# Kernel optimization log

Hardware: AMD Instinct MI355X
Metric: run time of the kernel (lower is better)

## Reference

```python
import jax, jax.numpy as jnp
import numpy as np

NEG_SLOPE = 0.2  # PyG GATConv leaky_relu slope


def _gat_layer(x, src, dst, W, a_src, a_dst, b, concat, num_nodes):
    # x: [N, F_in], W: [F_in, H*C], a_src/a_dst: [H, C], b: [H*C] or [C]
    H, C = a_src.shape
    h = (x @ W).reshape(num_nodes, H, C)                      # [N, H, C]
    s_src = jnp.einsum('nhc,hc->nh', h, a_src)                # [N, H]
    s_dst = jnp.einsum('nhc,hc->nh', h, a_dst)                # [N, H]
    e = jax.nn.leaky_relu(s_src[src] + s_dst[dst], NEG_SLOPE) # [E, H]
    # segment softmax over edges sharing a destination node
    m = jax.ops.segment_max(e, dst, num_segments=num_nodes)
    m = jnp.where(jnp.isfinite(m), m, 0.0)
    p = jnp.exp(e - m[dst])
    z = jax.ops.segment_sum(p, dst, num_segments=num_nodes)
    alpha = p / (z[dst] + 1e-16)                              # [E, H]
    msg = h[src] * alpha[:, :, None]                          # [E, H, C]
    out = jax.ops.segment_sum(msg, dst, num_segments=num_nodes)  # [N, H, C]
    out = out.reshape(num_nodes, H * C) if concat else out.mean(axis=1)
    return out + b


def setup_inputs() -> dict:
    key = jax.random.key(0)
    ks = jax.random.split(key, 16)
    N, E, F = 100000, 800000, 128
    H, C = 4, 32
    sc_in = 1.0 / np.sqrt(F)
    inp = {
        'x': jax.random.normal(ks[0], (N, F), jnp.float32),
        'edge_index': jax.random.randint(ks[1], (2, E), 0, N, jnp.int64),
        'W1': jax.random.normal(ks[2], (F, H * C), jnp.float32) * sc_in,
        'a_src1': jax.random.normal(ks[3], (H, C), jnp.float32),
        'a_dst1': jax.random.normal(ks[4], (H, C), jnp.float32),
        'b1': jax.random.normal(ks[5], (H * C,), jnp.float32) * 0.01,
        'W2': jax.random.normal(ks[6], (F, H * C), jnp.float32) * sc_in,
        'a_src2': jax.random.normal(ks[7], (H, C), jnp.float32),
        'a_dst2': jax.random.normal(ks[8], (H, C), jnp.float32),
        'b2': jax.random.normal(ks[9], (H * C,), jnp.float32) * 0.01,
        'W3': jax.random.normal(ks[10], (F, H * F), jnp.float32) * sc_in,
        'a_src3': jax.random.normal(ks[11], (H, F), jnp.float32),
        'a_dst3': jax.random.normal(ks[12], (H, F), jnp.float32),
        'b3': jax.random.normal(ks[13], (F,), jnp.float32) * 0.01,
    }
    return inp


def reference(x, edge_index, W1, a_src1, a_dst1, b1, W2, a_src2, a_dst2, b2,
              W3, a_src3, a_dst3, b3):
    N = x.shape[0]
    # PyG GATConv default: add self loops
    loop = jnp.arange(N, dtype=edge_index.dtype)
    src = jnp.concatenate([edge_index[0], loop])
    dst = jnp.concatenate([edge_index[1], loop])
    # conv1 (concat heads) + residual + ELU
    x1 = jax.nn.elu(_gat_layer(x, src, dst, W1, a_src1, a_dst1, b1, True, N) + x)
    # intermediate conv (concat heads) + residual + ELU
    x2 = jax.nn.elu(_gat_layer(x1, src, dst, W2, a_src2, a_dst2, b2, True, N) + x1)
    # final conv (mean over heads) + residual, no ELU
    x3 = _gat_layer(x2, src, dst, W3, a_src3, a_dst3, b3, False, N) + x2
    return x3
```

## Files before the change

kernel.cpp:

```cpp
#include <hip/hip_runtime.h>
#include <hip/hip_bf16.h>
#include <cstdint>

#define NEG_SLOPE 0.2f

typedef __bf16 bf16x8 __attribute__((ext_vector_type(8)));
typedef _Float16 half8 __attribute__((ext_vector_type(8)));
typedef float  floatx4 __attribute__((ext_vector_type(4)));

__device__ __forceinline__ float us2f(unsigned short u) {
    union { unsigned int i; float f; } c; c.i = ((unsigned int)u) << 16; return c.f;
}
__device__ __forceinline__ unsigned short f2us(float f) {
    union { float f; unsigned int i; } c; c.f = f;
    unsigned int x = c.i;
    unsigned int r = (x + 0x7fffu + ((x >> 16) & 1u)) >> 16;
    return (unsigned short)r;
}
__device__ __forceinline__ unsigned short f2h(float f) {
    union { _Float16 h; unsigned short u; } c; c.h = (_Float16)f; return c.u;
}
__device__ __forceinline__ float h2f(unsigned short u) {
    union { _Float16 h; unsigned short u; } c; c.u = u; return (float)c.h;
}
__device__ __forceinline__ float ldx(const void* p, int i, int bf) {
    return bf ? us2f(((const unsigned short*)p)[i]) : ((const float*)p)[i];
}
__device__ __forceinline__ void split2(float f, unsigned short& h, unsigned short& l) {
    h = f2us(f);
    l = f2us(f - us2f(h));
}
__device__ __forceinline__ float sel4(const float* a, int i) {
    float lo = (i & 1) ? a[1] : a[0];
    float hi = (i & 1) ? a[3] : a[2];
    return (i & 2) ? hi : lo;
}
__device__ __forceinline__ void unp8(uint4 u, float* f) {
    union { unsigned int i; float ff; } a;
    a.i = u.x << 16;          f[0] = a.ff;
    a.i = u.x & 0xffff0000u;  f[1] = a.ff;
    a.i = u.y << 16;          f[2] = a.ff;
    a.i = u.y & 0xffff0000u;  f[3] = a.ff;
    a.i = u.z << 16;          f[4] = a.ff;
    a.i = u.z & 0xffff0000u;  f[5] = a.ff;
    a.i = u.w << 16;          f[6] = a.ff;
    a.i = u.w & 0xffff0000u;  f[7] = a.ff;
}

__global__ void k_detect(const unsigned short* __restrict__ x16,
                         const unsigned int* __restrict__ ei,
                         int* __restrict__ flags) {
    if (threadIdx.x == 0 && blockIdx.x == 0) {
        int cnt = 0;
        for (int i = 0; i < 1024; ++i) {
            const unsigned short u = x16[2 * i];
            const int e = (u >> 7) & 0xFF;
            if (e < 100 || e > 160) ++cnt;
        }
        flags[0] = (cnt < 256) ? 1 : 0;
        int is64 = 1;
        for (int i = 0; i < 64; ++i)
            if (ei[2 * i + 1] != 0u) { is64 = 0; break; }
        flags[1] = is64;
    }
}

__device__ __forceinline__ int edge_at(const void* ei, int f64, long long idx) {
    if (f64) return (int)((const long long*)ei)[idx];
    return ((const int*)ei)[idx];
}

__global__ void k_hist(const void* __restrict__ ei, const int* __restrict__ flags,
                       int* __restrict__ deg, int E, int N) {
    const int f64 = flags[1];
    const int EP = E + N;
    for (int e = blockIdx.x * blockDim.x + threadIdx.x; e < EP; e += gridDim.x * blockDim.x) {
        int dst = (e < E) ? edge_at(ei, f64, (long long)E + e) : (e - E);
        atomicAdd(&deg[dst], 1);
    }
}

__global__ __launch_bounds__(1024) void k_scan_a(const int* __restrict__ deg,
                                                 int* __restrict__ coff,
                                                 int* __restrict__ part, int N) {
    __shared__ int tmp[1024];
    const int t = threadIdx.x, idx = blockIdx.x * 1024 + t;
    const int v = (idx < N) ? deg[idx] : 0;
    tmp[t] = v; __syncthreads();
    for (int s = 1; s < 1024; s <<= 1) {
        int a = (t >= s) ? tmp[t - s] : 0;
        __syncthreads(); tmp[t] += a; __syncthreads();
    }
    if (idx < N) coff[idx] = tmp[t] - v;
    if (t == 1023) part[blockIdx.x] = tmp[1023];
}

__global__ __launch_bounds__(1024) void k_scan_b(int* __restrict__ part,
                                                 int* __restrict__ coff, int nblk, int N) {
    __shared__ int tmp[1024];
    const int t = threadIdx.x;
    const int v = (t < nblk) ? part[t] : 0;
    tmp[t] = v; __syncthreads();
    for (int s = 1; s < 1024; s <<= 1) {
        int a = (t >= s) ? tmp[t - s] : 0;
        __syncthreads(); tmp[t] += a; __syncthreads();
    }
    if (t < nblk) part[t] = tmp[t] - v;
    if (t == 1023) coff[N] = tmp[1023];
}

__global__ __launch_bounds__(1024) void k_scan_c(int* __restrict__ coff,
                                                 const int* __restrict__ part, int N) {
    const int idx = blockIdx.x * 1024 + threadIdx.x;
    if (idx < N) coff[idx] += part[blockIdx.x];
}

__global__ void k_scatter(const void* __restrict__ ei, const int* __restrict__ flags,
                          const int* __restrict__ coff, int* __restrict__ cpos,
                          int* __restrict__ csrc, int E, int N) {
    const int f64 = flags[1];
    const int EP = E + N;
    for (int e = blockIdx.x * blockDim.x + threadIdx.x; e < EP; e += gridDim.x * blockDim.x) {
        int src, dst;
        if (e < E) { src = edge_at(ei, f64, e); dst = edge_at(ei, f64, (long long)E + e); }
        else       { src = dst = e - E; }
        const int p = atomicAdd(&cpos[dst], 1);
        csrc[coff[dst] + p] = src;
    }
}

template <int F16>
__global__ void k_wfrag(const void* __restrict__ Wv, const int* __restrict__ flags,
                        int wstride, int total,
                        unsigned short* __restrict__ outH, unsigned short* __restrict__ outL) {
    const int bf = flags[0];
    for (int tid = blockIdx.x * blockDim.x + threadIdx.x; tid < total;
         tid += gridDim.x * blockDim.x) {
        const int j    = tid & 7;
        const int lane = (tid >> 3) & 63;
        const int ks   = (tid >> 9) & 3;
        const int ntg  = (tid >> 11) & 7;
        const int blk  = tid >> 14;
        const int k = ks * 32 + (lane >> 4) * 8 + j;
        const int c = blk * 128 + ntg * 16 + (lane & 15);
        const float v = ldx(Wv, k * wstride + c, bf);
        unsigned short h, l;
        if (F16) {
            h = f2h(v);
            l = f2h(v - h2f(h));
        } else {
            split2(v, h, l);
        }
        outH[tid] = h; outL[tid] = l;
    }
}

__global__ void k_wa(const void* __restrict__ W, const void* __restrict__ as,
                     const void* __restrict__ ad, const int* __restrict__ flags,
                     float* __restrict__ va) {
    const int bf = flags[0];
    const int t = blockIdx.x * blockDim.x + threadIdx.x;
    if (t >= 512) return;
    const int k = t >> 2, h = t & 3;
    float ss = 0.f, dd = 0.f;
    for (int c = 0; c < 128; ++c) {
        const float w = ldx(W, k * 512 + h * 128 + c, bf);
        ss = fmaf(w, ldx(as, h * 128 + c, bf), ss);
        dd = fmaf(w, ldx(ad, h * 128 + c, bf), dd);
    }
    va[k * 8 + h] = ss;
    va[k * 8 + 4 + h] = dd;
}

template <bool XRAW, int SC>
__global__ __launch_bounds__(256) void k_gemm(const void* __restrict__ Xv,
                                              const unsigned short* __restrict__ whfB,
                                              const unsigned short* __restrict__ wlfB,
                                              unsigned short* __restrict__ Y16, int ystride,
                                              float* __restrict__ ssrc,
                                              float* __restrict__ sdst,
                                              const void* __restrict__ a_src,
                                              const void* __restrict__ a_dst,
                                              const int* __restrict__ flags,
                                              int N) {
    __shared__ __align__(16) unsigned short Ah[64][136], Al[64][136];
    __shared__ float sred[2][4][SC ? 64 : 1];
    const int bf   = flags[0];
    const int t    = threadIdx.x;
    const int row0 = blockIdx.x * 64;
    const int hy   = blockIdx.y;
    const unsigned short* whf = whfB + hy * 16384;
    const unsigned short* wlf = wlfB + hy * 16384;
    const int ycol0 = hy * 128;
    const int wv   = t >> 6;
    const int lane = t & 63;
    const int quad = lane >> 4;
    const int l16  = lane & 15;

#pragma unroll
    for (int it = 0; it < 8; ++it) {
        const int id = it * 256 + t;
        const int r  = id >> 5;
        const int c  = (id & 31) * 4;
        const int gr = row0 + r;
        ushort4 h4 = make_ushort4(0, 0, 0, 0), l4 = make_ushort4(0, 0, 0, 0);
        if (gr < N) {
            if (XRAW && bf) {
                h4 = *(const ushort4*)&((const unsigned short*)Xv)[(size_t)gr * 128 + c];
            } else {
                const float4 f = *(const float4*)&((const float*)Xv)[(size_t)gr * 128 + c];
                split2(f.x, h4.x, l4.x); split2(f.y, h4.y, l4.y);
                split2(f.z, h4.z, l4.z); split2(f.w, h4.w, l4.w);
            }
        }
        *(ushort4*)&Ah[r][c] = h4;
        *(ushort4*)&Al[r][c] = l4;
    }
    __syncthreads();

    floatx4 acc[4][2];
#pragma unroll
    for (int mt = 0; mt < 4; ++mt)
#pragma unroll
        for (int nt = 0; nt < 2; ++nt) acc[mt][nt] = (floatx4){0.f, 0.f, 0.f, 0.f};

#pragma unroll
    for (int ks = 0; ks < 4; ++ks) {
        const int ko = ks * 32 + quad * 8;
        bf16x8 ah[4], al[4], bh[2], bl[2];
#pragma unroll
        for (int mt = 0; mt < 4; ++mt) ah[mt] = *(const bf16x8*)&Ah[mt * 16 + l16][ko];
        if (!(XRAW && bf)) {
#pragma unroll
            for (int mt = 0; mt < 4; ++mt) al[mt] = *(const bf16x8*)&Al[mt * 16 + l16][ko];
        }
#pragma unroll
        for (int nt = 0; nt < 2; ++nt)
            bh[nt] = *(const bf16x8*)&whf[(((wv * 2 + nt) * 4 + ks) * 64 + lane) * 8];
        if (!bf) {
#pragma unroll
            for (int nt = 0; nt < 2; ++nt)
                bl[nt] = *(const bf16x8*)&wlf[(((wv * 2 + nt) * 4 + ks) * 64 + lane) * 8];
        }
#pragma unroll
        for (int mt = 0; mt < 4; ++mt)
#pragma unroll
            for (int nt = 0; nt < 2; ++nt) {
                acc[mt][nt] = __builtin_amdgcn_mfma_f32_16x16x32_bf16(ah[mt], bh[nt], acc[mt][nt], 0, 0, 0);
                if (!bf)
                    acc[mt][nt] = __builtin_amdgcn_mfma_f32_16x16x32_bf16(ah[mt], bl[nt], acc[mt][nt], 0, 0, 0);
                if (!(XRAW && bf))
                    acc[mt][nt] = __builtin_amdgcn_mfma_f32_16x16x32_bf16(al[mt], bh[nt], acc[mt][nt], 0, 0, 0);
            }
    }

    const int aBase = hy * 128 + wv * 32;
    float as_[2], ad_[2];
#pragma unroll
    for (int nt = 0; nt < 2; ++nt) {
        as_[nt] = ldx(a_src, aBase + nt * 16 + l16, bf);
        ad_[nt] = ldx(a_dst, aBase + nt * 16 + l16, bf);
    }

#pragma unroll
    for (int mt = 0; mt < 4; ++mt) {
        const int rl = mt * 16 + quad * 4;
#pragma unroll
        for (int r = 0; r < 4; ++r) {
            const int grow = row0 + rl + r;
            if (grow < N) {
#pragma unroll
                for (int nt = 0; nt < 2; ++nt)
                    Y16[(size_t)grow * ystride + ycol0 + wv * 32 + nt * 16 + l16] =
                        f2us(acc[mt][nt][r]);
            }
            float ps = acc[mt][0][r] * as_[0] + acc[mt][1][r] * as_[1];
            float pd = acc[mt][0][r] * ad_[0] + acc[mt][1][r] * ad_[1];
#pragma unroll
            for (int mk = 1; mk <= 8; mk <<= 1) {
                ps += __shfl_xor(ps, mk);
                pd += __shfl_xor(pd, mk);
            }
            if (SC == 0) {
                if (l16 == 0 && grow < N) {
                    ssrc[(size_t)grow * 4 + wv] = ps;
                    sdst[(size_t)grow * 4 + wv] = pd;
                }
            } else {
                if (l16 == 0) { sred[0][wv][rl + r] = ps; sred[1][wv][rl + r] = pd; }
            }
        }
    }
    if (SC == 1) {
        __syncthreads();
        if (t < 64 && row0 + t < N) {
            ssrc[(size_t)(row0 + t) * 4 + hy] = sred[0][0][t] + sred[0][1][t] + sred[0][2][t] + sred[0][3][t];
            sdst[(size_t)(row0 + t) * 4 + hy] = sred[1][0][t] + sred[1][1][t] + sred[1][2][t] + sred[1][3][t];
        }
    }
}

template <int MODE>
__global__ __launch_bounds__(256) void k_agg(const int* __restrict__ coff,
                                             const int* __restrict__ csrc,
                                             const float* __restrict__ ssrc,
                                             const float* __restrict__ sdst,
                                             const unsigned short* __restrict__ H16,
                                             const void* __restrict__ bias,
                                             const void* __restrict__ resid,
                                             const int* __restrict__ flags,
                                             void* __restrict__ out, int N,
                                             const float* __restrict__ va,
                                             float* __restrict__ ss2,
                                             float* __restrict__ sd2,
                                             unsigned short* __restrict__ x2h) {
    __shared__ float vaS[(MODE == 1) ? 128 : 1][10];
    const int bf   = flags[0];
    const int t    = threadIdx.x;
    const int l16  = t & 15;
    const int n0   = blockIdx.x * 16 + (t >> 4);
    const bool nact = n0 < N;
    const int n    = nact ? n0 : (N - 1);
    const int beg = coff[n], end = coff[n + 1];
    const int deg = end - beg;

    if (MODE == 1) {
        for (int i = t; i < 1024; i += 256) vaS[i >> 3][i & 7] = va[i];
        __syncthreads();
    }

    const float4 sdv = *(const float4*)&sdst[(size_t)n * 4];
    const float sd[4] = { sdv.x, sdv.y, sdv.z, sdv.w };
    const bool fast = (deg <= 16);
    float z[4];
    int   myS = 0;
    float wn[4] = { 0.f, 0.f, 0.f, 0.f };

    if (fast) {
        const bool act = l16 < deg;
        if (act) {
            myS = csrc[beg + l16];
            const float4 sp = *(const float4*)&ssrc[(size_t)myS * 4];
            const float s4[4] = { sp.x, sp.y, sp.z, sp.w };
#pragma unroll
            for (int h = 0; h < 4; ++h) {
                float tv = s4[h] + sd[h];
                tv = tv >= 0.f ? tv : NEG_SLOPE * tv;
                wn[h] = __expf(fminf(tv, 80.f));
            }
        }
#pragma unroll
        for (int h = 0; h < 4; ++h) z[h] = wn[h];
#pragma unroll
        for (int mk = 1; mk <= 8; mk <<= 1)
#pragma unroll
            for (int h = 0; h < 4; ++h) z[h] += __shfl_xor(z[h], mk);
    } else {
#pragma unroll
        for (int h = 0; h < 4; ++h) z[h] = 0.f;
        for (int e = beg + l16; e < end; e += 16) {
            const int s = csrc[e];
            const float4 sp = *(const float4*)&ssrc[(size_t)s * 4];
            const float s4[4] = { sp.x, sp.y, sp.z, sp.w };
#pragma unroll
            for (int h = 0; h < 4; ++h) {
                float tv = s4[h] + sd[h];
                tv = tv >= 0.f ? tv : NEG_SLOPE * tv;
                z[h] += __expf(fminf(tv, 80.f));
            }
        }
#pragma unroll
        for (int mk = 1; mk <= 8; mk <<= 1)
#pragma unroll
            for (int h = 0; h < 4; ++h) z[h] += __shfl_xor(z[h], mk);
    }

    float ivz[4];
#pragma unroll
    for (int h = 0; h < 4; ++h) ivz[h] = 1.f / (z[h] + 1e-16f);

    const int c8 = l16 * 8;
    const int hd = l16 >> 2;
    const float ih = sel4(ivz, hd);
    float ac[8];
#pragma unroll
    for (int j = 0; j < 8; ++j) ac[j] = 0.f;

    if (fast) {
        for (int e = 0; e < deg; ++e) {
            const int s = __shfl(myS, e, 16);
            float wa4[4];
            wa4[0] = __shfl(wn[0], e, 16);
            wa4[1] = __shfl(wn[1], e, 16);
            wa4[2] = __shfl(wn[2], e, 16);
            wa4[3] = __shfl(wn[3], e, 16);
            const float w = sel4(wa4, hd);
            const uint4 u = *(const uint4*)&H16[(size_t)s * 128 + c8];
            float f[8]; unp8(u, f);
#pragma unroll
            for (int j = 0; j < 8; ++j) ac[j] = fmaf(w, f[j], ac[j]);
        }
    } else {
        const float sdh = sel4(sd, hd);
        for (int e = beg; e < end; ++e) {
            const int s = csrc[e];
            float tv = ssrc[(size_t)s * 4 + hd] + sdh;
            tv = tv >= 0.f ? tv : NEG_SLOPE * tv;
            const float w = __expf(fminf(tv, 80.f));
            const uint4 u = *(const uint4*)&H16[(size_t)s * 128 + c8];
            float f[8]; unp8(u, f);
#pragma unroll
            for (int j = 0; j < 8; ++j) ac[j] = fmaf(w, f[j], ac[j]);
        }
    }

#pragma unroll
    for (int j = 0; j < 8; ++j) ac[j] *= ih;

    if (!nact) return;
    const int ob = n * 128 + c8;
    float rr[8];
    if (MODE == 0) {
        if (bf) {
            const uint4 u = *(const uint4*)&((const unsigned short*)resid)[ob];
            unp8(u, rr);
        } else {
            const float4 r0 = *(const float4*)&((const float*)resid)[ob];
            const float4 r1 = *(const float4*)&((const float*)resid)[ob + 4];
            rr[0] = r0.x; rr[1] = r0.y; rr[2] = r0.z; rr[3] = r0.w;
            rr[4] = r1.x; rr[5] = r1.y; rr[6] = r1.z; rr[7] = r1.w;
        }
    } else {
        const float4 r0 = *(const float4*)&((const float*)resid)[ob];
        const float4 r1 = *(const float4*)&((const float*)resid)[ob + 4];
        rr[0] = r0.x; rr[1] = r0.y; rr[2] = r0.z; rr[3] = r0.w;
        rr[4] = r1.x; rr[5] = r1.y; rr[6] = r1.z; rr[7] = r1.w;
    }
    float o[8];
#pragma unroll
    for (int j = 0; j < 8; ++j) {
        const float v = ac[j] + ldx(bias, c8 + j, bf) + rr[j];
        o[j] = v > 0.f ? v : expm1f(v);
    }
    *(float4*)&((float*)out)[ob]     = make_float4(o[0], o[1], o[2], o[3]);
    *(float4*)&((float*)out)[ob + 4] = make_float4(o[4], o[5], o[6], o[7]);

    if (MODE == 1) {
        uint4 u16;
        u16.x = (unsigned int)f2us(o[0]) | ((unsigned int)f2us(o[1]) << 16);
        u16.y = (unsigned int)f2us(o[2]) | ((unsigned int)f2us(o[3]) << 16);
        u16.z = (unsigned int)f2us(o[4]) | ((unsigned int)f2us(o[5]) << 16);
        u16.w = (unsigned int)f2us(o[6]) | ((unsigned int)f2us(o[7]) << 16);
        *(uint4*)&x2h[ob] = u16;
        float p[8];
#pragma unroll
        for (int o8 = 0; o8 < 8; ++o8) {
            float acc = 0.f;
#pragma unroll
            for (int j = 0; j < 8; ++j) acc = fmaf(o[j], vaS[c8 + j][o8], acc);
            p[o8] = acc;
        }
#pragma unroll
        for (int mk = 1; mk <= 8; mk <<= 1)
#pragma unroll
            for (int o8 = 0; o8 < 8; ++o8) p[o8] += __shfl_xor(p[o8], mk);
        if (l16 == 0) {
#pragma unroll
            for (int h = 0; h < 4; ++h) {
                ss2[(size_t)n * 4 + h] = p[h];
                sd2[(size_t)n * 4 + h] = p[4 + h];
            }
        }
    }
}

__global__ __launch_bounds__(256) void k_aggx(const int* __restrict__ coff,
                                              const int* __restrict__ csrc,
                                              const float* __restrict__ ssrc,
                                              const float* __restrict__ sdst,
                                              const unsigned short* __restrict__ X16,
                                              unsigned short* __restrict__ aggO,
                                              int N) {
    const int t    = threadIdx.x;
    const int l16  = t & 15;
    const int n0   = blockIdx.x * 16 + (t >> 4);
    const bool nact = n0 < N;
    const int n    = nact ? n0 : (N - 1);
    const int beg = coff[n], end = coff[n + 1];
    const int deg = end - beg;

    const float4 sdv = *(const float4*)&sdst[(size_t)n * 4];
    const float sd[4] = { sdv.x, sdv.y, sdv.z, sdv.w };
    const bool fast = (deg <= 16);
    float m[4], z[4];
    int   myS = 0;
    float wn[4] = { 0.f, 0.f, 0.f, 0.f };

    if (fast) {
        const bool act = l16 < deg;
        float v[4];
#pragma unroll
        for (int h = 0; h < 4; ++h) v[h] = -1e30f;
        if (act) {
            myS = csrc[beg + l16];
            const float4 sp = *(const float4*)&ssrc[(size_t)myS * 4];
            const float s4[4] = { sp.x, sp.y, sp.z, sp.w };
#pragma unroll
            for (int h = 0; h < 4; ++h) {
                float tv = s4[h] + sd[h];
                v[h] = tv >= 0.f ? tv : NEG_SLOPE * tv;
            }
        }
#pragma unroll
        for (int h = 0; h < 4; ++h) m[h] = v[h];
#pragma unroll
        for (int mk = 1; mk <= 8; mk <<= 1)
#pragma unroll
            for (int h = 0; h < 4; ++h) m[h] = fmaxf(m[h], __shfl_xor(m[h], mk));
        float w[4];
#pragma unroll
        for (int h = 0; h < 4; ++h) w[h] = act ? __expf(v[h] - m[h]) : 0.f;
#pragma unroll
        for (int h = 0; h < 4; ++h) z[h] = w[h];
#pragma unroll
        for (int mk = 1; mk <= 8; mk <<= 1)
#pragma unroll
            for (int h = 0; h < 4; ++h) z[h] += __shfl_xor(z[h], mk);
#pragma unroll
        for (int h = 0; h < 4; ++h) wn[h] = w[h] / (z[h] + 1e-16f);
    } else {
#pragma unroll
        for (int h = 0; h < 4; ++h) m[h] = -1e30f;
        for (int e = beg + l16; e < end; e += 16) {
            const int s = csrc[e];
            const float4 sp = *(const float4*)&ssrc[(size_t)s * 4];
            const float s4[4] = { sp.x, sp.y, sp.z, sp.w };
#pragma unroll
            for (int h = 0; h < 4; ++h) {
                float tv = s4[h] + sd[h];
                tv = tv >= 0.f ? tv : NEG_SLOPE * tv;
                m[h] = fmaxf(m[h], tv);
            }
        }
#pragma unroll
        for (int mk = 1; mk <= 8; mk <<= 1)
#pragma unroll
            for (int h = 0; h < 4; ++h) m[h] = fmaxf(m[h], __shfl_xor(m[h], mk));
#pragma unroll
        for (int h = 0; h < 4; ++h) z[h] = 0.f;
        for (int e = beg + l16; e < end; e += 16) {
            const int s = csrc[e];
            const float4 sp = *(const float4*)&ssrc[(size_t)s * 4];
            const float s4[4] = { sp.x, sp.y, sp.z, sp.w };
#pragma unroll
            for (int h = 0; h < 4; ++h) {
                float tv = s4[h] + sd[h];
                tv = tv >= 0.f ? tv : NEG_SLOPE * tv;
                z[h] += __expf(tv - m[h]);
            }
        }
#pragma unroll
        for (int mk = 1; mk <= 8; mk <<= 1)
#pragma unroll
            for (int h = 0; h < 4; ++h) z[h] += __shfl_xor(z[h], mk);
    }

    const int c8 = l16 * 8;
    float ac[4][8];
#pragma unroll
    for (int h = 0; h < 4; ++h)
#pragma unroll
        for (int j = 0; j < 8; ++j) ac[h][j] = 0.f;

    if (fast) {
        int e = 0;
        for (; e + 2 <= deg; e += 2) {
            const int s0 = __shfl(myS, e + 0, 16);
            const int s1 = __shfl(myS, e + 1, 16);
            const uint4 u0 = *(const uint4*)&X16[(size_t)s0 * 128 + c8];
            const uint4 u1 = *(const uint4*)&X16[(size_t)s1 * 128 + c8];
            float w0[4], w1[4];
#pragma unroll
            for (int h = 0; h < 4; ++h) {
                w0[h] = __shfl(wn[h], e + 0, 16);
                w1[h] = __shfl(wn[h], e + 1, 16);
            }
            float f[8];
            unp8(u0, f);
#pragma unroll
            for (int h = 0; h < 4; ++h)
#pragma unroll
                for (int j = 0; j < 8; ++j) ac[h][j] = fmaf(w0[h], f[j], ac[h][j]);
            unp8(u1, f);
#pragma unroll
            for (int h = 0; h < 4; ++h)
#pragma unroll
                for (int j = 0; j < 8; ++j) ac[h][j] = fmaf(w1[h], f[j], ac[h][j]);
        }
        for (; e < deg; ++e) {
            const int s = __shfl(myS, e, 16);
            float wr[4];
            wr[0] = __shfl(wn[0], e, 16);
            wr[1] = __shfl(wn[1], e, 16);
            wr[2] = __shfl(wn[2], e, 16);
            wr[3] = __shfl(wn[3], e, 16);
            const uint4 u = *(const uint4*)&X16[(size_t)s * 128 + c8];
            float f[8]; unp8(u, f);
#pragma unroll
            for (int h = 0; h < 4; ++h)
#pragma unroll
                for (int j = 0; j < 8; ++j) ac[h][j] = fmaf(wr[h], f[j], ac[h][j]);
        }
    } else {
        float ivh[4];
#pragma unroll
        for (int h = 0; h < 4; ++h) ivh[h] = 1.f / (z[h] + 1e-16f);
        for (int e = beg; e < end; ++e) {
            const int s = csrc[e];
            const float4 sp = *(const float4*)&ssrc[(size_t)s * 4];
            const float s4[4] = { sp.x, sp.y, sp.z, sp.w };
            float wr[4];
#pragma unroll
            for (int h = 0; h < 4; ++h) {
                float tv = s4[h] + sd[h];
                tv = tv >= 0.f ? tv : NEG_SLOPE * tv;
                wr[h] = __expf(tv - m[h]) * ivh[h];
            }
            const uint4 u = *(const uint4*)&X16[(size_t)s * 128 + c8];
            float f[8]; unp8(u, f);
#pragma unroll
            for (int h = 0; h < 4; ++h)
#pragma unroll
                for (int j = 0; j < 8; ++j) ac[h][j] = fmaf(wr[h], f[j], ac[h][j]);
        }
    }

    if (!nact) return;
#pragma unroll
    for (int h = 0; h < 4; ++h) {
        uint4 u;
        u.x = (unsigned int)f2h(ac[h][0]) | ((unsigned int)f2h(ac[h][1]) << 16);
        u.y = (unsigned int)f2h(ac[h][2]) | ((unsigned int)f2h(ac[h][3]) << 16);
        u.z = (unsigned int)f2h(ac[h][4]) | ((unsigned int)f2h(ac[h][5]) << 16);
        u.w = (unsigned int)f2h(ac[h][6]) | ((unsigned int)f2h(ac[h][7]) << 16);
        *(uint4*)&aggO[(size_t)n0 * 512 + h * 128 + c8] = u;
    }
}

__global__ __launch_bounds__(256) void k_gemm3(const unsigned short* __restrict__ A16,
                                               const unsigned short* __restrict__ whf,
                                               const unsigned short* __restrict__ wlf,
                                               const void* __restrict__ bias,
                                               const float* __restrict__ resid,
                                               const int* __restrict__ flags,
                                               void* __restrict__ out, int N) {
    __shared__ __align__(16) unsigned short Ah[64][136];
    const int bf   = flags[0];
    const int t    = threadIdx.x;
    const int row0 = blockIdx.x * 64;
    const int wv   = t >> 6;
    const int lane = t & 63;
    const int quad = lane >> 4;
    const int l16  = lane & 15;

    floatx4 acc[4][2];
#pragma unroll
    for (int mt = 0; mt < 4; ++mt)
#pragma unroll
        for (int nt = 0; nt < 2; ++nt) acc[mt][nt] = (floatx4){0.f, 0.f, 0.f, 0.f};

    for (int kc = 0; kc < 4; ++kc) {
        if (kc) __syncthreads();
#pragma unroll
        for (int it = 0; it < 8; ++it) {
            const int id = it * 256 + t;
            const int r  = id >> 5;
            const int c  = (id & 31) * 4;
            ushort4 h4 = make_ushort4(0, 0, 0, 0);
            if (row0 + r < N)
                h4 = *(const ushort4*)&A16[(size_t)(row0 + r) * 512 + kc * 128 + c];
            *(ushort4*)&Ah[r][c] = h4;
        }
        __syncthreads();

        const unsigned short* whc = whf + kc * 16384;
        const unsigned short* wlc = wlf + kc * 16384;
#pragma unroll
        for (int ks = 0; ks < 4; ++ks) {
            const int ko = ks * 32 + quad * 8;
            half8 ah[4], bh[2], bl[2];
#pragma unroll
            for (int mt = 0; mt < 4; ++mt) ah[mt] = *(const half8*)&Ah[mt * 16 + l16][ko];
#pragma unroll
            for (int nt = 0; nt < 2; ++nt) {
                bh[nt] = *(const half8*)&whc[(((wv * 2 + nt) * 4 + ks) * 64 + lane) * 8];
                bl[nt] = *(const half8*)&wlc[(((wv * 2 + nt) * 4 + ks) * 64 + lane) * 8];
            }
#pragma unroll
            for (int mt = 0; mt < 4; ++mt)
#pragma unroll
                for (int nt = 0; nt < 2; ++nt) {
                    acc[mt][nt] = __builtin_amdgcn_mfma_f32_16x16x32_f16(ah[mt], bh[nt], acc[mt][nt], 0, 0, 0);
                    acc[mt][nt] = __builtin_amdgcn_mfma_f32_16x16x32_f16(ah[mt], bl[nt], acc[mt][nt], 0, 0, 0);
                }
        }
    }

#pragma unroll
    for (int mt = 0; mt < 4; ++mt) {
        const int rl = mt * 16 + quad * 4;
#pragma unroll
        for (int r = 0; r < 4; ++r) {
            const int grow = row0 + rl + r;
            if (grow < N) {
#pragma unroll
                for (int nt = 0; nt < 2; ++nt) {
                    const int col = wv * 32 + nt * 16 + l16;
                    const float v = acc[mt][nt][r] * 0.25f + ldx(bias, col, bf)
                                  + resid[(size_t)grow * 128 + col];
                    if (bf) ((unsigned short*)out)[(size_t)grow * 128 + col] = f2us(v);
                    else    ((float*)out)[(size_t)grow * 128 + col] = v;
                }
            }
        }
    }
}

extern "C" void kernel_launch(void* const* d_in, const int* in_sizes, int n_in,
                              void* d_out, int out_size, void* d_ws, size_t ws_size,
                              hipStream_t stream) {
    const int N  = in_sizes[0] / 128;
    const int E  = in_sizes[1] / 2;
    const int EP = E + N;

    const void* x   = d_in[0];
    const void* ei  = d_in[1];
    const void* W1  = d_in[2];
    const void* as1 = d_in[3];
    const void* ad1 = d_in[4];
    const void* b1  = d_in[5];
    const void* W2  = d_in[6];
    const void* as2 = d_in[7];
    const void* ad2 = d_in[8];
    const void* b2  = d_in[9];
    const void* W3  = d_in[10];
    const void* as3 = d_in[11];
    const void* ad3 = d_in[12];
    const void* b3  = d_in[13];

    char* p = (char*)d_ws;
    auto alloc = [&](size_t bytes) { char* r = p; p += (bytes + 255) & ~(size_t)255; return r; };
    int*   flags = (int*)alloc(8);
    int*   deg   = (int*)alloc((size_t)(N + 1) * 4);
    int*   coff  = (int*)alloc((size_t)(N + 1) * 4);
    int*   cpos  = (int*)alloc((size_t)N * 4);
    int*   part  = (int*)alloc(4096);
    int*   csrc  = (int*)alloc((size_t)EP * 4);
    char*  region = alloc((size_t)N * 512 * 2);
    float* x2b   = (float*)alloc((size_t)N * 128 * 4);
    float* ssrc  = (float*)alloc((size_t)N * 4 * 4);
    float* sdst  = (float*)alloc((size_t)N * 4 * 4);
    unsigned short* whf1 = (unsigned short*)alloc(16384 * 2);
    unsigned short* wlf1 = (unsigned short*)alloc(16384 * 2);
    unsigned short* whf2 = (unsigned short*)alloc(16384 * 2);
    unsigned short* wlf2 = (unsigned short*)alloc(16384 * 2);
    unsigned short* whf3 = (unsigned short*)alloc(65536 * 2);
    unsigned short* wlf3 = (unsigned short*)alloc(65536 * 2);
    unsigned short* x2h  = (unsigned short*)alloc((size_t)N * 128 * 2);
    float* va    = (float*)alloc(128 * 8 * 4);
    float* ssrc3 = (float*)alloc((size_t)N * 4 * 4);
    float* sdst3 = (float*)alloc((size_t)N * 4 * 4);

    float*          x1b    = (float*)region;
    unsigned short* h16_12 = (unsigned short*)(region + (size_t)N * 128 * 4);
    unsigned short* aggF   = (unsigned short*)region;

    hipMemsetAsync(deg,  0, (size_t)(N + 1) * 4, stream);
    hipMemsetAsync(cpos, 0, (size_t)N * 4, stream);

    k_detect<<<1, 64, 0, stream>>>((const unsigned short*)x, (const unsigned int*)ei, flags);

    k_wfrag<0><<<64, 256, 0, stream>>>(W1, flags, 128, 16384, whf1, wlf1);
    k_wfrag<0><<<64, 256, 0, stream>>>(W2, flags, 128, 16384, whf2, wlf2);
    k_wfrag<1><<<256, 256, 0, stream>>>(W3, flags, 512, 65536, whf3, wlf3);
    k_wa<<<2, 256, 0, stream>>>(W3, as3, ad3, flags, va);

    const int egrid = (EP + 255) / 256;
    const int nblk  = (N + 1023) / 1024;
    k_hist<<<egrid, 256, 0, stream>>>(ei, flags, deg, E, N);
    k_scan_a<<<nblk, 1024, 0, stream>>>(deg, coff, part, N);
    k_scan_b<<<1, 1024, 0, stream>>>(part, coff, nblk, N);
    k_scan_c<<<nblk, 1024, 0, stream>>>(coff, part, N);
    k_scatter<<<egrid, 256, 0, stream>>>(ei, flags, coff, cpos, csrc, E, N);

    const int ggrid = (N + 63) / 64;
    const int ngrid = (N + 15) / 16;

    k_gemm<true, 0><<<dim3(ggrid, 1), 256, 0, stream>>>(x, whf1, wlf1, h16_12, 128,
                                                        ssrc, sdst, as1, ad1, flags, N);
    k_agg<0><<<ngrid, 256, 0, stream>>>(coff, csrc, ssrc, sdst, h16_12, b1, x, flags, x1b, N,
                                        nullptr, nullptr, nullptr, nullptr);

    k_gemm<false, 0><<<dim3(ggrid, 1), 256, 0, stream>>>(x1b, whf2, wlf2, h16_12, 128,
                                                         ssrc, sdst, as2, ad2, flags, N);
    k_agg<1><<<ngrid, 256, 0, stream>>>(coff, csrc, ssrc, sdst, h16_12, b2, x1b, flags, x2b, N,
                                        va, ssrc3, sdst3, x2h);

    k_aggx<<<ngrid, 256, 0, stream>>>(coff, csrc, ssrc3, sdst3, x2h, aggF, N);
    k_gemm3<<<ggrid, 256, 0, stream>>>(aggF, whf3, wlf3, b3, x2b, flags, d_out, N);
}
```

Measured before the change: 670.3 us.

## Fuse layer-3 aggregation with head-projection GEMM via shared-memory staging

The third-layer aggregation and the following GEMM are merged into one kernel. Each block aggregates 32 nodes into an fp16 shared-memory tile and then runs the MFMA projection straight from LDS, so the N x 512 fp16 intermediate no longer goes through global memory. The fp32 x2 residual buffer is replaced by a bf16 hi/lo split pair, which cuts the layer-2 write and layer-3 residual read from 4 to 4 bytes per element in two arrays, keeping near-fp32 accuracy. The trade-off is a smaller GEMM tile of 32 rows per block, which re-reads the weight fragments more often, and lower occupancy from the large LDS tile.

```diff
diff --git a/kernel.cpp b/kernel.cpp
--- a/kernel.cpp
+++ b/kernel.cpp
@@ -313,7 +313,8 @@
                                              const float* __restrict__ va,
                                              float* __restrict__ ss2,
                                              float* __restrict__ sd2,
-                                             unsigned short* __restrict__ x2h) {
+                                             unsigned short* __restrict__ x2h,
+                                             unsigned short* __restrict__ x2l) {
     __shared__ float vaS[(MODE == 1) ? 128 : 1][10];
     const int bf   = flags[0];
     const int t    = threadIdx.x;
@@ -442,16 +443,29 @@
         const float v = ac[j] + ldx(bias, c8 + j, bf) + rr[j];
         o[j] = v > 0.f ? v : expm1f(v);
     }
-    *(float4*)&((float*)out)[ob]     = make_float4(o[0], o[1], o[2], o[3]);
-    *(float4*)&((float*)out)[ob + 4] = make_float4(o[4], o[5], o[6], o[7]);
+    if (MODE == 0) {
+        *(float4*)&((float*)out)[ob]     = make_float4(o[0], o[1], o[2], o[3]);
+        *(float4*)&((float*)out)[ob + 4] = make_float4(o[4], o[5], o[6], o[7]);
+    }
 
     if (MODE == 1) {
-        uint4 u16;
-        u16.x = (unsigned int)f2us(o[0]) | ((unsigned int)f2us(o[1]) << 16);
-        u16.y = (unsigned int)f2us(o[2]) | ((unsigned int)f2us(o[3]) << 16);
-        u16.z = (unsigned int)f2us(o[4]) | ((unsigned int)f2us(o[5]) << 16);
-        u16.w = (unsigned int)f2us(o[6]) | ((unsigned int)f2us(o[7]) << 16);
-        *(uint4*)&x2h[ob] = u16;
+        unsigned short hi[8], lo[8];
+#pragma unroll
+        for (int j = 0; j < 8; ++j) {
+            hi[j] = f2us(o[j]);
+            lo[j] = f2us(o[j] - us2f(hi[j]));
+        }
+        uint4 uh, ul;
+        uh.x = (unsigned int)hi[0] | ((unsigned int)hi[1] << 16);
+        uh.y = (unsigned int)hi[2] | ((unsigned int)hi[3] << 16);
+        uh.z = (unsigned int)hi[4] | ((unsigned int)hi[5] << 16);
+        uh.w = (unsigned int)hi[6] | ((unsigned int)hi[7] << 16);
+        ul.x = (unsigned int)lo[0] | ((unsigned int)lo[1] << 16);
+        ul.y = (unsigned int)lo[2] | ((unsigned int)lo[3] << 16);
+        ul.z = (unsigned int)lo[4] | ((unsigned int)lo[5] << 16);
+        ul.w = (unsigned int)lo[6] | ((unsigned int)lo[7] << 16);
+        *(uint4*)&x2h[ob] = uh;
+        *(uint4*)&x2l[ob] = ul;
         float p[8];
 #pragma unroll
         for (int o8 = 0; o8 < 8; ++o8) {
@@ -474,230 +488,216 @@
     }
 }
 
-__global__ __launch_bounds__(256) void k_aggx(const int* __restrict__ coff,
-                                              const int* __restrict__ csrc,
-                                              const float* __restrict__ ssrc,
-                                              const float* __restrict__ sdst,
-                                              const unsigned short* __restrict__ X16,
-                                              unsigned short* __restrict__ aggO,
-                                              int N) {
-    const int t    = threadIdx.x;
-    const int l16  = t & 15;
-    const int n0   = blockIdx.x * 16 + (t >> 4);
-    const bool nact = n0 < N;
-    const int n    = nact ? n0 : (N - 1);
-    const int beg = coff[n], end = coff[n + 1];
-    const int deg = end - beg;
-
-    const float4 sdv = *(const float4*)&sdst[(size_t)n * 4];
-    const float sd[4] = { sdv.x, sdv.y, sdv.z, sdv.w };
-    const bool fast = (deg <= 16);
-    float m[4], z[4];
-    int   myS = 0;
-    float wn[4] = { 0.f, 0.f, 0.f, 0.f };
-
-    if (fast) {
-        const bool act = l16 < deg;
-        float v[4];
-#pragma unroll
-        for (int h = 0; h < 4; ++h) v[h] = -1e30f;
-        if (act) {
-            myS = csrc[beg + l16];
-            const float4 sp = *(const float4*)&ssrc[(size_t)myS * 4];
-            const float s4[4] = { sp.x, sp.y, sp.z, sp.w };
-#pragma unroll
-            for (int h = 0; h < 4; ++h) {
-                float tv = s4[h] + sd[h];
-                v[h] = tv >= 0.f ? tv : NEG_SLOPE * tv;
-            }
-        }
-#pragma unroll
-        for (int h = 0; h < 4; ++h) m[h] = v[h];
-#pragma unroll
-        for (int mk = 1; mk <= 8; mk <<= 1)
-#pragma unroll
-            for (int h = 0; h < 4; ++h) m[h] = fmaxf(m[h], __shfl_xor(m[h], mk));
-        float w[4];
-#pragma unroll
-        for (int h = 0; h < 4; ++h) w[h] = act ? __expf(v[h] - m[h]) : 0.f;
-#pragma unroll
-        for (int h = 0; h < 4; ++h) z[h] = w[h];
-#pragma unroll
-        for (int mk = 1; mk <= 8; mk <<= 1)
-#pragma unroll
-            for (int h = 0; h < 4; ++h) z[h] += __shfl_xor(z[h], mk);
-#pragma unroll
-        for (int h = 0; h < 4; ++h) wn[h] = w[h] / (z[h] + 1e-16f);
-    } else {
-#pragma unroll
-        for (int h = 0; h < 4; ++h) m[h] = -1e30f;
-        for (int e = beg + l16; e < end; e += 16) {
-            const int s = csrc[e];
-            const float4 sp = *(const float4*)&ssrc[(size_t)s * 4];
-            const float s4[4] = { sp.x, sp.y, sp.z, sp.w };
-#pragma unroll
-            for (int h = 0; h < 4; ++h) {
-                float tv = s4[h] + sd[h];
-                tv = tv >= 0.f ? tv : NEG_SLOPE * tv;
-                m[h] = fmaxf(m[h], tv);
-            }
-        }
-#pragma unroll
-        for (int mk = 1; mk <= 8; mk <<= 1)
-#pragma unroll
-            for (int h = 0; h < 4; ++h) m[h] = fmaxf(m[h], __shfl_xor(m[h], mk));
-#pragma unroll
-        for (int h = 0; h < 4; ++h) z[h] = 0.f;
-        for (int e = beg + l16; e < end; e += 16) {
-            const int s = csrc[e];
-            const float4 sp = *(const float4*)&ssrc[(size_t)s * 4];
-            const float s4[4] = { sp.x, sp.y, sp.z, sp.w };
-#pragma unroll
-            for (int h = 0; h < 4; ++h) {
-                float tv = s4[h] + sd[h];
-                tv = tv >= 0.f ? tv : NEG_SLOPE * tv;
-                z[h] += __expf(tv - m[h]);
-            }
-        }
-#pragma unroll
-        for (int mk = 1; mk <= 8; mk <<= 1)
-#pragma unroll
-            for (int h = 0; h < 4; ++h) z[h] += __shfl_xor(z[h], mk);
-    }
-
-    const int c8 = l16 * 8;
-    float ac[4][8];
-#pragma unroll
-    for (int h = 0; h < 4; ++h)
-#pragma unroll
-        for (int j = 0; j < 8; ++j) ac[h][j] = 0.f;
-
-    if (fast) {
-        int e = 0;
-        for (; e + 2 <= deg; e += 2) {
-            const int s0 = __shfl(myS, e + 0, 16);
-            const int s1 = __shfl(myS, e + 1, 16);
-            const uint4 u0 = *(const uint4*)&X16[(size_t)s0 * 128 + c8];
-            const uint4 u1 = *(const uint4*)&X16[(size_t)s1 * 128 + c8];
-            float w0[4], w1[4];
-#pragma unroll
-            for (int h = 0; h < 4; ++h) {
-                w0[h] = __shfl(wn[h], e + 0, 16);
-                w1[h] = __shfl(wn[h], e + 1, 16);
-            }
-            float f[8];
-            unp8(u0, f);
-#pragma unroll
-            for (int h = 0; h < 4; ++h)
-#pragma unroll
-                for (int j = 0; j < 8; ++j) ac[h][j] = fmaf(w0[h], f[j], ac[h][j]);
-            unp8(u1, f);
-#pragma unroll
-            for (int h = 0; h < 4; ++h)
-#pragma unroll
-                for (int j = 0; j < 8; ++j) ac[h][j] = fmaf(w1[h], f[j], ac[h][j]);
-        }
-        for (; e < deg; ++e) {
-            const int s = __shfl(myS, e, 16);
-            float wr[4];
-            wr[0] = __shfl(wn[0], e, 16);
-            wr[1] = __shfl(wn[1], e, 16);
-            wr[2] = __shfl(wn[2], e, 16);
-            wr[3] = __shfl(wn[3], e, 16);
-            const uint4 u = *(const uint4*)&X16[(size_t)s * 128 + c8];
-            float f[8]; unp8(u, f);
-#pragma unroll
-            for (int h = 0; h < 4; ++h)
-#pragma unroll
-                for (int j = 0; j < 8; ++j) ac[h][j] = fmaf(wr[h], f[j], ac[h][j]);
-        }
-    } else {
-        float ivh[4];
-#pragma unroll
-        for (int h = 0; h < 4; ++h) ivh[h] = 1.f / (z[h] + 1e-16f);
-        for (int e = beg; e < end; ++e) {
-            const int s = csrc[e];
-            const float4 sp = *(const float4*)&ssrc[(size_t)s * 4];
-            const float s4[4] = { sp.x, sp.y, sp.z, sp.w };
-            float wr[4];
-#pragma unroll
-            for (int h = 0; h < 4; ++h) {
-                float tv = s4[h] + sd[h];
-                tv = tv >= 0.f ? tv : NEG_SLOPE * tv;
-                wr[h] = __expf(tv - m[h]) * ivh[h];
-            }
-            const uint4 u = *(const uint4*)&X16[(size_t)s * 128 + c8];
-            float f[8]; unp8(u, f);
-#pragma unroll
-            for (int h = 0; h < 4; ++h)
-#pragma unroll
-                for (int j = 0; j < 8; ++j) ac[h][j] = fmaf(wr[h], f[j], ac[h][j]);
-        }
-    }
-
-    if (!nact) return;
-#pragma unroll
-    for (int h = 0; h < 4; ++h) {
-        uint4 u;
-        u.x = (unsigned int)f2h(ac[h][0]) | ((unsigned int)f2h(ac[h][1]) << 16);
-        u.y = (unsigned int)f2h(ac[h][2]) | ((unsigned int)f2h(ac[h][3]) << 16);
-        u.z = (unsigned int)f2h(ac[h][4]) | ((unsigned int)f2h(ac[h][5]) << 16);
-        u.w = (unsigned int)f2h(ac[h][6]) | ((unsigned int)f2h(ac[h][7]) << 16);
-        *(uint4*)&aggO[(size_t)n0 * 512 + h * 128 + c8] = u;
-    }
-}
-
-__global__ __launch_bounds__(256) void k_gemm3(const unsigned short* __restrict__ A16,
+__global__ __launch_bounds__(256) void k_aggx3(const int* __restrict__ coff,
+                                               const int* __restrict__ csrc,
+                                               const float* __restrict__ ssrc,
+                                               const float* __restrict__ sdst,
+                                               const unsigned short* __restrict__ X16,
+                                               const unsigned short* __restrict__ Xl16,
                                                const unsigned short* __restrict__ whf,
                                                const unsigned short* __restrict__ wlf,
                                                const void* __restrict__ bias,
-                                               const float* __restrict__ resid,
                                                const int* __restrict__ flags,
                                                void* __restrict__ out, int N) {
-    __shared__ __align__(16) unsigned short Ah[64][136];
+    __shared__ __align__(16) unsigned short aggS[4][32][136];
     const int bf   = flags[0];
     const int t    = threadIdx.x;
-    const int row0 = blockIdx.x * 64;
+    const int row0 = blockIdx.x * 32;
+    const int l16  = t & 15;
+
+    for (int sb = 0; sb < 2; ++sb) {
+        const int r  = sb * 16 + (t >> 4);
+        const int n0 = row0 + r;
+        const int n  = (n0 < N) ? n0 : (N - 1);
+        const int beg = coff[n], end = coff[n + 1];
+        const int deg = end - beg;
+
+        const float4 sdv = *(const float4*)&sdst[(size_t)n * 4];
+        const float sd[4] = { sdv.x, sdv.y, sdv.z, sdv.w };
+        const bool fast = (deg <= 16);
+        float m[4], z[4];
+        int   myS = 0;
+        float wn[4] = { 0.f, 0.f, 0.f, 0.f };
+
+        if (fast) {
+            const bool act = l16 < deg;
+            float v[4];
+#pragma unroll
+            for (int h = 0; h < 4; ++h) v[h] = -1e30f;
+            if (act) {
+                myS = csrc[beg + l16];
+                const float4 sp = *(const float4*)&ssrc[(size_t)myS * 4];
+                const float s4[4] = { sp.x, sp.y, sp.z, sp.w };
+#pragma unroll
+                for (int h = 0; h < 4; ++h) {
+                    float tv = s4[h] + sd[h];
+                    v[h] = tv >= 0.f ? tv : NEG_SLOPE * tv;
+                }
+            }
+#pragma unroll
+            for (int h = 0; h < 4; ++h) m[h] = v[h];
+#pragma unroll
+            for (int mk = 1; mk <= 8; mk <<= 1)
+#pragma unroll
+                for (int h = 0; h < 4; ++h) m[h] = fmaxf(m[h], __shfl_xor(m[h], mk));
+            float w[4];
+#pragma unroll
+            for (int h = 0; h < 4; ++h) w[h] = act ? __expf(v[h] - m[h]) : 0.f;
+#pragma unroll
+            for (int h = 0; h < 4; ++h) z[h] = w[h];
+#pragma unroll
+            for (int mk = 1; mk <= 8; mk <<= 1)
+#pragma unroll
+                for (int h = 0; h < 4; ++h) z[h] += __shfl_xor(z[h], mk);
+#pragma unroll
+            for (int h = 0; h < 4; ++h) wn[h] = w[h] / (z[h] + 1e-16f);
+        } else {
+#pragma unroll
+            for (int h = 0; h < 4; ++h) m[h] = -1e30f;
+            for (int e = beg + l16; e < end; e += 16) {
+                const int s = csrc[e];
+                const float4 sp = *(const float4*)&ssrc[(size_t)s * 4];
+                const float s4[4] = { sp.x, sp.y, sp.z, sp.w };
+#pragma unroll
+                for (int h = 0; h < 4; ++h) {
+                    float tv = s4[h] + sd[h];
+                    tv = tv >= 0.f ? tv : NEG_SLOPE * tv;
+                    m[h] = fmaxf(m[h], tv);
+                }
+            }
+#pragma unroll
+            for (int mk = 1; mk <= 8; mk <<= 1)
+#pragma unroll
+                for (int h = 0; h < 4; ++h) m[h] = fmaxf(m[h], __shfl_xor(m[h], mk));
+#pragma unroll
+            for (int h = 0; h < 4; ++h) z[h] = 0.f;
+            for (int e = beg + l16; e < end; e += 16) {
+                const int s = csrc[e];
+                const float4 sp = *(const float4*)&ssrc[(size_t)s * 4];
+                const float s4[4] = { sp.x, sp.y, sp.z, sp.w };
+#pragma unroll
+                for (int h = 0; h < 4; ++h) {
+                    float tv = s4[h] + sd[h];
+                    tv = tv >= 0.f ? tv : NEG_SLOPE * tv;
+                    z[h] += __expf(tv - m[h]);
+                }
+            }
+#pragma unroll
+            for (int mk = 1; mk <= 8; mk <<= 1)
+#pragma unroll
+                for (int h = 0; h < 4; ++h) z[h] += __shfl_xor(z[h], mk);
+        }
+
+        const int c8 = l16 * 8;
+        float ac[4][8];
+#pragma unroll
+        for (int h = 0; h < 4; ++h)
+#pragma unroll
+            for (int j = 0; j < 8; ++j) ac[h][j] = 0.f;
+
+        if (fast) {
+            int e = 0;
+            for (; e + 2 <= deg; e += 2) {
+                const int s0 = __shfl(myS, e + 0, 16);
+                const int s1 = __shfl(myS, e + 1, 16);
+                const uint4 u0 = *(const uint4*)&X16[(size_t)s0 * 128 + c8];
+                const uint4 u1 = *(const uint4*)&X16[(size_t)s1 * 128 + c8];
+                float w0[4], w1[4];
+#pragma unroll
+                for (int h = 0; h < 4; ++h) {
+                    w0[h] = __shfl(wn[h], e + 0, 16);
+                    w1[h] = __shfl(wn[h], e + 1, 16);
+                }
+                float f[8];
+                unp8(u0, f);
+#pragma unroll
+                for (int h = 0; h < 4; ++h)
+#pragma unroll
+                    for (int j = 0; j < 8; ++j) ac[h][j] = fmaf(w0[h], f[j], ac[h][j]);
+                unp8(u1, f);
+#pragma unroll
+                for (int h = 0; h < 4; ++h)
+#pragma unroll
+                    for (int j = 0; j < 8; ++j) ac[h][j] = fmaf(w1[h], f[j], ac[h][j]);
+            }
+            for (; e < deg; ++e) {
+                const int s = __shfl(myS, e, 16);
+                float wr[4];
+                wr[0] = __shfl(wn[0], e, 16);
+                wr[1] = __shfl(wn[1], e, 16);
+                wr[2] = __shfl(wn[2], e, 16);
+                wr[3] = __shfl(wn[3], e, 16);
+                const uint4 u = *(const uint4*)&X16[(size_t)s * 128 + c8];
+                float f[8]; unp8(u, f);
+#pragma unroll
+                for (int h = 0; h < 4; ++h)
+#pragma unroll
+                    for (int j = 0; j < 8; ++j) ac[h][j] = fmaf(wr[h], f[j], ac[h][j]);
+            }
+        } else {
+            float ivh[4];
+#pragma unroll
+            for (int h = 0; h < 4; ++h) ivh[h] = 1.f / (z[h] + 1e-16f);
+            for (int e = beg; e < end; ++e) {
+                const int s = csrc[e];
+                const float4 sp = *(const float4*)&ssrc[(size_t)s * 4];
+                const float s4[4] = { sp.x, sp.y, sp.z, sp.w };
+                float wr[4];
+#pragma unroll
+                for (int h = 0; h < 4; ++h) {
+                    float tv = s4[h] + sd[h];
+                    tv = tv >= 0.f ? tv : NEG_SLOPE * tv;
+                    wr[h] = __expf(tv - m[h]) * ivh[h];
+                }
+                const uint4 u = *(const uint4*)&X16[(size_t)s * 128 + c8];
+                float f[8]; unp8(u, f);
+#pragma unroll
+                for (int h = 0; h < 4; ++h)
+#pragma unroll
+                    for (int j = 0; j < 8; ++j) ac[h][j] = fmaf(wr[h], f[j], ac[h][j]);
+            }
+        }
+
+#pragma unroll
+        for (int h = 0; h < 4; ++h) {
+            uint4 u;
+            u.x = (unsigned int)f2h(ac[h][0]) | ((unsigned int)f2h(ac[h][1]) << 16);
+            u.y = (unsigned int)f2h(ac[h][2]) | ((unsigned int)f2h(ac[h][3]) << 16);
+            u.z = (unsigned int)f2h(ac[h][4]) | ((unsigned int)f2h(ac[h][5]) << 16);
+            u.w = (unsigned int)f2h(ac[h][6]) | ((unsigned int)f2h(ac[h][7]) << 16);
+            *(uint4*)&aggS[h][r][c8] = u;
+        }
+    }
+    __syncthreads();
+
     const int wv   = t >> 6;
     const int lane = t & 63;
     const int quad = lane >> 4;
-    const int l16  = lane & 15;
-
-    floatx4 acc[4][2];
-#pragma unroll
-    for (int mt = 0; mt < 4; ++mt)
+    const int q16  = lane & 15;
+
+    floatx4 acc[2][2];
+#pragma unroll
+    for (int mt = 0; mt < 2; ++mt)
 #pragma unroll
         for (int nt = 0; nt < 2; ++nt) acc[mt][nt] = (floatx4){0.f, 0.f, 0.f, 0.f};
 
+#pragma unroll
     for (int kc = 0; kc < 4; ++kc) {
-        if (kc) __syncthreads();
-#pragma unroll
-        for (int it = 0; it < 8; ++it) {
-            const int id = it * 256 + t;
-            const int r  = id >> 5;
-            const int c  = (id & 31) * 4;
-            ushort4 h4 = make_ushort4(0, 0, 0, 0);
-            if (row0 + r < N)
-                h4 = *(const ushort4*)&A16[(size_t)(row0 + r) * 512 + kc * 128 + c];
-            *(ushort4*)&Ah[r][c] = h4;
-        }
-        __syncthreads();
-
         const unsigned short* whc = whf + kc * 16384;
         const unsigned short* wlc = wlf + kc * 16384;
 #pragma unroll
         for (int ks = 0; ks < 4; ++ks) {
             const int ko = ks * 32 + quad * 8;
-            half8 ah[4], bh[2], bl[2];
-#pragma unroll
-            for (int mt = 0; mt < 4; ++mt) ah[mt] = *(const half8*)&Ah[mt * 16 + l16][ko];
+            half8 ah[2], bh[2], bl[2];
+#pragma unroll
+            for (int mt = 0; mt < 2; ++mt) ah[mt] = *(const half8*)&aggS[kc][mt * 16 + q16][ko];
 #pragma unroll
             for (int nt = 0; nt < 2; ++nt) {
                 bh[nt] = *(const half8*)&whc[(((wv * 2 + nt) * 4 + ks) * 64 + lane) * 8];
                 bl[nt] = *(const half8*)&wlc[(((wv * 2 + nt) * 4 + ks) * 64 + lane) * 8];
             }
 #pragma unroll
-            for (int mt = 0; mt < 4; ++mt)
+            for (int mt = 0; mt < 2; ++mt)
 #pragma unroll
                 for (int nt = 0; nt < 2; ++nt) {
                     acc[mt][nt] = __builtin_amdgcn_mfma_f32_16x16x32_f16(ah[mt], bh[nt], acc[mt][nt], 0, 0, 0);
@@ -707,7 +707,7 @@
     }
 
 #pragma unroll
-    for (int mt = 0; mt < 4; ++mt) {
+    for (int mt = 0; mt < 2; ++mt) {
         const int rl = mt * 16 + quad * 4;
 #pragma unroll
         for (int r = 0; r < 4; ++r) {
@@ -715,11 +715,12 @@
             if (grow < N) {
 #pragma unroll
                 for (int nt = 0; nt < 2; ++nt) {
-                    const int col = wv * 32 + nt * 16 + l16;
-                    const float v = acc[mt][nt][r] * 0.25f + ldx(bias, col, bf)
-                                  + resid[(size_t)grow * 128 + col];
-                    if (bf) ((unsigned short*)out)[(size_t)grow * 128 + col] = f2us(v);
-                    else    ((float*)out)[(size_t)grow * 128 + col] = v;
+                    const int col = wv * 32 + nt * 16 + q16;
+                    const size_t ix = (size_t)grow * 128 + col;
+                    const float resid = us2f(X16[ix]) + us2f(Xl16[ix]);
+                    const float v = acc[mt][nt][r] * 0.25f + ldx(bias, col, bf) + resid;
+                    if (bf) ((unsigned short*)out)[ix] = f2us(v);
+                    else    ((float*)out)[ix] = v;
                 }
             }
         }
@@ -756,8 +757,8 @@
     int*   cpos  = (int*)alloc((size_t)N * 4);
     int*   part  = (int*)alloc(4096);
     int*   csrc  = (int*)alloc((size_t)EP * 4);
-    char*  region = alloc((size_t)N * 512 * 2);
-    float* x2b   = (float*)alloc((size_t)N * 128 * 4);
+    float* x1b   = (float*)alloc((size_t)N * 128 * 4);
+    unsigned short* h16_12 = (unsigned short*)alloc((size_t)N * 128 * 2);
     float* ssrc  = (float*)alloc((size_t)N * 4 * 4);
     float* sdst  = (float*)alloc((size_t)N * 4 * 4);
     unsigned short* whf1 = (unsigned short*)alloc(16384 * 2);
@@ -767,13 +768,10 @@
     unsigned short* whf3 = (unsigned short*)alloc(65536 * 2);
     unsigned short* wlf3 = (unsigned short*)alloc(65536 * 2);
     unsigned short* x2h  = (unsigned short*)alloc((size_t)N * 128 * 2);
+    unsigned short* x2l  = (unsigned short*)alloc((size_t)N * 128 * 2);
     float* va    = (float*)alloc(128 * 8 * 4);
     float* ssrc3 = (float*)alloc((size_t)N * 4 * 4);
     float* sdst3 = (float*)alloc((size_t)N * 4 * 4);
-
-    float*          x1b    = (float*)region;
-    unsigned short* h16_12 = (unsigned short*)(region + (size_t)N * 128 * 4);
-    unsigned short* aggF   = (unsigned short*)region;
 
     hipMemsetAsync(deg,  0, (size_t)(N + 1) * 4, stream);
     hipMemsetAsync(cpos, 0, (size_t)N * 4, stream);
@@ -795,17 +793,18 @@
 
     const int ggrid = (N + 63) / 64;
     const int ngrid = (N + 15) / 16;
+    const int fgrid = (N + 31) / 32;
 
     k_gemm<true, 0><<<dim3(ggrid, 1), 256, 0, stream>>>(x, whf1, wlf1, h16_12, 128,
                                                         ssrc, sdst, as1, ad1, flags, N);
     k_agg<0><<<ngrid, 256, 0, stream>>>(coff, csrc, ssrc, sdst, h16_12, b1, x, flags, x1b, N,
-                                        nullptr, nullptr, nullptr, nullptr);
+                                        nullptr, nullptr, nullptr, nullptr, nullptr);
 
     k_gemm<false, 0><<<dim3(ggrid, 1), 256, 0, stream>>>(x1b, whf2, wlf2, h16_12, 128,
                                                          ssrc, sdst, as2, ad2, flags, N);
-    k_agg<1><<<ngrid, 256, 0, stream>>>(coff, csrc, ssrc, sdst, h16_12, b2, x1b, flags, x2b, N,
-                                        va, ssrc3, sdst3, x2h);
-
-    k_aggx<<<ngrid, 256, 0, stream>>>(coff, csrc, ssrc3, sdst3, x2h, aggF, N);
-    k_gemm3<<<ggrid, 256, 0, stream>>>(aggF, whf3, wlf3, b3, x2b, flags, d_out, N);
-}
+    k_agg<1><<<ngrid, 256, 0, stream>>>(coff, csrc, ssrc, sdst, h16_12, b2, x1b, flags, nullptr, N,
+                                        va, ssrc3, sdst3, x2h, x2l);
+
+    k_aggx3<<<fgrid, 256, 0, stream>>>(coff, csrc, ssrc3, sdst3, x2h, x2l,
+                                       whf3, wlf3, b3, flags, d_out, N);
+}
```

Measured after the change: 636.0 us. 1.05x faster.
